# Kernel optimization log

Hardware: AMD Instinct MI355X
Metric: run time of the kernel (lower is better)

## Reference

```python
import jax, jax.numpy as jnp
import numpy as np

B, S, E, NH = 4, 1024, 512, 8
D = E // NH

def layer_norm(x, scale, bias, eps=1e-5):
    mu = jnp.mean(x, -1, keepdims=True)
    var = jnp.mean((x - mu) ** 2, -1, keepdims=True)
    return (x - mu) * jax.lax.rsqrt(var + eps) * scale + bias

def mha(qx, kx, vx, qw, qb, kw, kb, vw, vb, ow, ob, temp):
    b, sq, e = qx.shape
    sk = kx.shape[1]
    q = (qx @ qw + qb).reshape(b, sq, NH, D)
    k = (kx @ kw + kb).reshape(b, sk, NH, D)
    v = (vx @ vw + vb).reshape(b, sk, NH, D)
    scores = jnp.einsum('bqhd,bkhd->bhqk', q, k) * (D ** -0.5) / temp
    w = jax.nn.softmax(scores, axis=-1)  # dropout is identity in eval mode
    o = jnp.einsum('bhqk,bkhd->bqhd', w, v).reshape(b, sq, e)
    return o @ ow + ob

def setup_inputs():
    key = jax.random.key(0)
    ks = jax.random.split(key, 10)
    sc = 0.02  # init scale for weights
    return {
        'body_feats': jax.random.normal(ks[0], (B, S, E), jnp.float32),
        'limb_feats': jax.random.normal(ks[1], (B, S, E), jnp.float32),
        'attn_qw': jax.random.normal(ks[2], (4, E, E), jnp.float32) * sc,
        'attn_qb': jnp.zeros((4, E), jnp.float32),
        'attn_kw': jax.random.normal(ks[3], (4, E, E), jnp.float32) * sc,
        'attn_kb': jnp.zeros((4, E), jnp.float32),
        'attn_vw': jax.random.normal(ks[4], (4, E, E), jnp.float32) * sc,
        'attn_vb': jnp.zeros((4, E), jnp.float32),
        'attn_ow': jax.random.normal(ks[5], (4, E, E), jnp.float32) * sc,
        'attn_ob': jnp.zeros((4, E), jnp.float32),
        'ffn_w1': jax.random.normal(ks[6], (2, E, 4 * E), jnp.float32) * sc,
        'ffn_b1': jnp.zeros((2, 4 * E), jnp.float32),
        'ffn_w2': jax.random.normal(ks[7], (2, 4 * E, E), jnp.float32) * sc,
        'ffn_b2': jnp.zeros((2, E), jnp.float32),
        'norm_scale': jnp.ones((6, E), jnp.float32),
        'norm_bias': jnp.zeros((6, E), jnp.float32),
        'gate_w': jax.random.normal(ks[8], (2 * E, 2), jnp.float32) * sc,
        'gate_b': jnp.zeros((2,), jnp.float32),
        'temperature': 1,
    }

def reference(body_feats, limb_feats, attn_qw, attn_qb, attn_kw, attn_kb, attn_vw, attn_vb, attn_ow, attn_ob, ffn_w1, ffn_b1, ffn_w2, ffn_b2, norm_scale, norm_bias, gate_w, gate_b, temperature):
    temp = jnp.float32(temperature)
    # attn index: 0=self_body 1=self_limb 2=body2limb 3=limb2body
    # norm index: 0=norm1_body 1=norm2_body 2=norm3_body 3=norm1_limb 4=norm2_limb 5=norm3_limb
    def attn(i, qx, kx, vx):
        return mha(qx, kx, vx, attn_qw[i], attn_qb[i], attn_kw[i], attn_kb[i], attn_vw[i], attn_vb[i], attn_ow[i], attn_ob[i], temp)
    def ffn(i, x):
        return jax.nn.gelu(x @ ffn_w1[i] + ffn_b1[i], approximate=False) @ ffn_w2[i] + ffn_b2[i]
    def ln(i, x):
        return layer_norm(x, norm_scale[i], norm_bias[i])
    body = ln(0, body_feats + attn(0, body_feats, body_feats, body_feats))
    limb = ln(3, limb_feats + attn(1, limb_feats, limb_feats, limb_feats))
    body_cross = attn(2, body, limb, limb)
    limb_cross = attn(3, limb, body, body)
    body_gate = jax.nn.softmax(jnp.concatenate([body, body_cross], -1) @ gate_w + gate_b, axis=-1)
    limb_gate = jax.nn.softmax(jnp.concatenate([limb, limb_cross], -1) @ gate_w + gate_b, axis=-1)
    # NOTE: original torch code applies norm2_body to BOTH streams (preserved faithfully)
    body = ln(1, body * body_gate[..., 0:1] + body_cross * body_gate[..., 1:2])
    limb = ln(1, limb * limb_gate[..., 0:1] + limb_cross * limb_gate[..., 1:2])
    body = ln(2, body + ffn(0, body))
    limb = ln(5, limb + ffn(1, limb))
    return body, limb
```

## Files before the change

kernel.cpp:

```cpp
#include <hip/hip_runtime.h>

#define AS1 __attribute__((address_space(1)))
#define AS3 __attribute__((address_space(3)))

typedef __attribute__((ext_vector_type(4))) float f32x4;
typedef __attribute__((ext_vector_type(8))) short s16x8;

static __device__ __forceinline__ ushort f2bf(float f) {
  union { float f; unsigned u; } x; x.f = f;
  unsigned r = x.u + 0x7FFFu + ((x.u >> 16) & 1u);
  return (ushort)(r >> 16);
}
static __device__ __forceinline__ float bf2f(ushort u) {
  union { unsigned u; float f; } x; x.u = ((unsigned)u) << 16; return x.f;
}
static __device__ __forceinline__ float ex2(float x) {
  return __builtin_amdgcn_exp2f(x);
}
static __device__ __forceinline__ float parse_scalar(const void* p) {
  int i = *(const int*)p;
  if (i > 0 && i < 1000000) return (float)i;
  union { int i; float f; } u; u.i = i; return u.f;
}

__global__ __launch_bounds__(256)
void transpose_all(const float* __restrict__ qw, const float* __restrict__ kw,
                   const float* __restrict__ vw, const float* __restrict__ ow,
                   const float* __restrict__ w1, const float* __restrict__ w2,
                   ushort* __restrict__ FW, ushort* __restrict__ WOT,
                   ushort* __restrict__ W1T, ushort* __restrict__ W2T)
{
  __shared__ float tile[32][33];
  int id = blockIdx.x;
  const float* in; ushort* out; int K, N, tx, ty;
  if (id < 3072) {
    int trip = id / 768, r = id - trip * 768, which = r >> 8, t2 = r & 255;
    int widx = (which == 0) ? trip : (trip ^ (trip >> 1));
    in = ((which == 0) ? qw : (which == 1) ? kw : vw) + (size_t)widx * 512 * 512;
    out = FW + (size_t)trip * 1536 * 512 + (size_t)which * 512 * 512;
    K = 512; N = 512; tx = t2 & 15; ty = t2 >> 4;
  } else if (id < 4096) {
    int r = id - 3072, wi = r >> 8, t2 = r & 255;
    in = ow + (size_t)wi * 512 * 512; out = WOT + (size_t)wi * 512 * 512;
    K = 512; N = 512; tx = t2 & 15; ty = t2 >> 4;
  } else if (id < 6144) {
    int r = id - 4096, s = r >> 10, t2 = r & 1023;
    in = w1 + (size_t)s * 512 * 2048; out = W1T + (size_t)s * 2048 * 512;
    K = 512; N = 2048; tx = t2 & 63; ty = t2 >> 6;
  } else {
    int r = id - 6144, s = r >> 10, t2 = r & 1023;
    in = w2 + (size_t)s * 2048 * 512; out = W2T + (size_t)s * 512 * 2048;
    K = 2048; N = 512; tx = t2 & 15; ty = t2 >> 4;
  }
  int nb = tx * 32, kb = ty * 32;
  int x = threadIdx.x, y = threadIdx.y;
  #pragma unroll
  for (int i = 0; i < 4; ++i)
    tile[y + i * 8][x] = in[(size_t)(kb + y + i * 8) * N + nb + x];
  __syncthreads();
  #pragma unroll
  for (int i = 0; i < 4; ++i)
    out[(size_t)(nb + y + i * 8) * K + kb + x] = f2bf(tile[x][y + i * 8]);
}

__global__ __launch_bounds__(256)
void cvt2_bf16(const float* __restrict__ a, const float* __restrict__ b,
               ushort* __restrict__ oa, ushort* __restrict__ ob)
{
  const float* in = blockIdx.y ? b : a;
  ushort* out = blockIdx.y ? ob : oa;
  int i = (blockIdx.x * 256 + threadIdx.x) * 4;
  float4 v = *(const float4*)(in + i);
  ushort4 o;
  o.x = f2bf(v.x); o.y = f2bf(v.y); o.z = f2bf(v.z); o.w = f2bf(v.w);
  *(ushort4*)(out + i) = o;
}

struct GemmArgs {
  const ushort* A; const ushort* Bt;
  const float *b0, *b1, *b2;
  float* outf; ushort* outb;
  ushort *qo, *ko, *vto;
  const void* sp;
  int M, N, K, kind;
};

template<int FM, int FN>
__global__ __launch_bounds__(256)
void gemm_k(GemmArgs g0, GemmArgs g1)
{
  constexpr int BM = FM * 32, BN = FN * 32;
  __shared__ ushort As[2][BM * 64];
  __shared__ ushort Bs[2][BN * 64];
  GemmArgs g = blockIdx.z ? g1 : g0;
  const int t = threadIdx.x, lane = t & 63, w = t >> 6;
  const int lr = lane & 15, gq = lane >> 4;
  const int wr = w >> 1, wc = w & 1;
  const int m0 = blockIdx.y * BM, n0 = blockIdx.x * BN;
  const int K = g.K;
  const int nk = K >> 6;

  auto stage = [&](int kt, int buf) {
    #pragma unroll
    for (int p = 0; p < FM; ++p) {
      int c = p * 256 + t, row = c >> 3, sl = c & 7;
      const ushort* src = g.A + (size_t)(m0 + row) * K + kt * 64 + ((sl ^ (row & 7)) << 3);
      __builtin_amdgcn_global_load_lds((const AS1 void*)src,
          (AS3 void*)(As[buf] + (size_t)(p * 256 + (t & ~63)) * 8), 16, 0, 0);
    }
    #pragma unroll
    for (int p = 0; p < FN; ++p) {
      int c = p * 256 + t, row = c >> 3, sl = c & 7;
      const ushort* src = g.Bt + (size_t)(n0 + row) * K + kt * 64 + ((sl ^ (row & 7)) << 3);
      __builtin_amdgcn_global_load_lds((const AS1 void*)src,
          (AS3 void*)(Bs[buf] + (size_t)(p * 256 + (t & ~63)) * 8), 16, 0, 0);
    }
  };

  f32x4 acc[FM][FN];
  f32x4 zero = {0.f, 0.f, 0.f, 0.f};
  #pragma unroll
  for (int m = 0; m < FM; ++m)
    #pragma unroll
    for (int n = 0; n < FN; ++n) acc[m][n] = zero;

  stage(0, 0);
  __syncthreads();
  for (int kt = 0; kt < nk; ++kt) {
    int cur = kt & 1;
    const ushort* Ab = As[cur];
    const ushort* Bb = Bs[cur];
    if (kt + 1 < nk) stage(kt + 1, cur ^ 1);
    #pragma unroll
    for (int ks = 0; ks < 2; ++ks) {
      s16x8 af[FM], bfv[FN];
      #pragma unroll
      for (int m = 0; m < FM; ++m) {
        int row = wr * (FM * 16) + m * 16 + lr;
        af[m] = *(const s16x8*)(Ab + row * 64 + (((ks * 4 + gq) ^ (row & 7)) << 3));
      }
      #pragma unroll
      for (int n = 0; n < FN; ++n) {
        int row = wc * (FN * 16) + n * 16 + lr;
        bfv[n] = *(const s16x8*)(Bb + row * 64 + (((ks * 4 + gq) ^ (row & 7)) << 3));
      }
      __builtin_amdgcn_s_setprio(1);
      #pragma unroll
      for (int m = 0; m < FM; ++m)
        #pragma unroll
        for (int n = 0; n < FN; ++n)
          acc[m][n] = __builtin_amdgcn_mfma_f32_16x16x32_bf16(af[m], bfv[n], acc[m][n], 0, 0, 0);
      __builtin_amdgcn_s_setprio(0);
    }
    __syncthreads();
  }

  float qs = 1.0f;
  if (g.kind == 3 && g.sp) qs = 0.125f / parse_scalar(g.sp) * 1.4426950408889634f;
  #pragma unroll
  for (int n = 0; n < FN; ++n) {
    int col = n0 + wc * (FN * 16) + n * 16 + lr;
    int seg = col >> 9, cm = col & 511;
    float bv;
    if (g.kind == 3) bv = (seg == 0) ? g.b0[cm] : (seg == 1) ? g.b1[cm] : g.b2[cm];
    else bv = g.b0 ? g.b0[col] : 0.f;
    #pragma unroll
    for (int m = 0; m < FM; ++m) {
      int rowb = m0 + wr * (FM * 16) + m * 16 + 4 * gq;
      if (g.kind == 3) {
        if (seg == 2) {
          int d = cm & 63, hh = cm >> 6, bb = rowb >> 10, s = rowb & 1023;
          ushort4 pk;
          pk.x = f2bf(acc[m][n][0] + bv); pk.y = f2bf(acc[m][n][1] + bv);
          pk.z = f2bf(acc[m][n][2] + bv); pk.w = f2bf(acc[m][n][3] + bv);
          *(ushort4*)(g.vto + (((size_t)(bb * 8 + hh) * 64 + d) << 10) + s) = pk;
        } else if (seg == 1) {
          #pragma unroll
          for (int r = 0; r < 4; ++r)
            g.ko[(size_t)(rowb + r) * 512 + cm] = f2bf(acc[m][n][r] + bv);
        } else {
          #pragma unroll
          for (int r = 0; r < 4; ++r)
            g.qo[(size_t)(rowb + r) * 512 + cm] = f2bf((acc[m][n][r] + bv) * qs);
        }
      } else {
        #pragma unroll
        for (int r = 0; r < 4; ++r) {
          float v = acc[m][n][r] + bv;
          if (g.kind == 2) v = 0.5f * v * (1.0f + erff(v * 0.70710678118654752f));
          if (g.kind == 0) g.outf[(size_t)(rowb + r) * g.N + col] = v;
          else g.outb[(size_t)(rowb + r) * g.N + col] = f2bf(v);
        }
      }
    }
  }
}

__global__ __launch_bounds__(256)
void attn_core(const ushort* __restrict__ Q0, const ushort* __restrict__ K0,
               const ushort* __restrict__ V0, ushort* __restrict__ O0,
               const ushort* __restrict__ Q1, const ushort* __restrict__ K1,
               const ushort* __restrict__ V1, ushort* __restrict__ O1)
{
  __shared__ ushort Ks[2][64 * 64];
  __shared__ ushort Vs[2][64 * 64];
  __shared__ ushort Ps[4][1024];
  const int str = blockIdx.y;
  const ushort* Q = str ? Q1 : Q0;
  const ushort* Kx = str ? K1 : K0;
  const ushort* VT = str ? V1 : V0;
  ushort* O = str ? O1 : O0;

  const int t = threadIdx.x, lane = t & 63, w = t >> 6;
  const int lr = lane & 15, g = lane >> 4;
  int bid = blockIdx.x;
  int L = (bid & 7) * 64 + (bid >> 3);
  int bh = L >> 4, qt = L & 15;
  size_t tbase = ((size_t)(bh >> 3) << 19) + ((size_t)(bh & 7) << 6);
  const ushort* Kbase = Kx + tbase;
  const ushort* Vbase = VT + ((size_t)bh << 16);
  int q0 = qt * 64 + w * 16;
  ushort* myPs = Ps[w];

  auto stage = [&](int kt, int buf) {
    #pragma unroll
    for (int p = 0; p < 2; ++p) {
      int c = p * 256 + t, row = c >> 3, sl = c & 7;
      const ushort* src = Kbase + (size_t)(kt * 64 + row) * 512 + ((sl ^ (row & 7)) << 3);
      __builtin_amdgcn_global_load_lds((const AS1 void*)src,
          (AS3 void*)(Ks[buf] + (size_t)(p * 256 + (t & ~63)) * 8), 16, 0, 0);
    }
    #pragma unroll
    for (int p = 0; p < 2; ++p) {
      int c = p * 256 + t, row = c >> 3, sl = c & 7;
      const ushort* src = Vbase + (size_t)row * 1024 + kt * 64 + ((sl ^ (row & 7)) << 3);
      __builtin_amdgcn_global_load_lds((const AS1 void*)src,
          (AS3 void*)(Vs[buf] + (size_t)(p * 256 + (t & ~63)) * 8), 16, 0, 0);
    }
  };

  s16x8 qf[2];
  #pragma unroll
  for (int ks = 0; ks < 2; ++ks)
    qf[ks] = *(const s16x8*)(Q + tbase + (size_t)(q0 + lr) * 512 + ks * 32 + g * 8);

  f32x4 po[4];
  f32x4 zero = {0.f, 0.f, 0.f, 0.f};
  #pragma unroll
  for (int dt = 0; dt < 4; ++dt) po[dt] = zero;
  float mrow[4] = {-1e30f, -1e30f, -1e30f, -1e30f};
  float lsum[4] = {0.f, 0.f, 0.f, 0.f};

  stage(0, 0);
  __syncthreads();
  #pragma unroll 2
  for (int kt = 0; kt < 16; ++kt) {
    int cur = kt & 1;
    const ushort* Kb = Ks[cur];
    const ushort* Vb = Vs[cur];
    if (kt < 15) stage(kt + 1, cur ^ 1);

    f32x4 sc[4];
    #pragma unroll
    for (int c = 0; c < 4; ++c) {
      sc[c] = zero;
      #pragma unroll
      for (int ks = 0; ks < 2; ++ks) {
        int row = c * 16 + lr;
        s16x8 kf = *(const s16x8*)(Kb + row * 64 + (((ks * 4 + g) ^ (row & 7)) << 3));
        sc[c] = __builtin_amdgcn_mfma_f32_16x16x32_bf16(qf[ks], kf, sc[c], 0, 0, 0);
      }
    }

    #pragma unroll
    for (int r = 0; r < 4; ++r) {
      float tm = fmaxf(fmaxf(sc[0][r], sc[1][r]), fmaxf(sc[2][r], sc[3][r]));
      #pragma unroll
      for (int msk = 1; msk < 16; msk <<= 1) tm = fmaxf(tm, __shfl_xor(tm, msk));
      float nm = fmaxf(mrow[r], tm);
      float fr = ex2(mrow[r] - nm);
      float ps = 0.f;
      #pragma unroll
      for (int c = 0; c < 4; ++c) {
        float pv = ex2(sc[c][r] - nm);
        sc[c][r] = pv;
        ps += pv;
      }
      #pragma unroll
      for (int msk = 1; msk < 16; msk <<= 1) ps += __shfl_xor(ps, msk);
      lsum[r] = lsum[r] * fr + ps;
      mrow[r] = nm;
      #pragma unroll
      for (int dt = 0; dt < 4; ++dt) po[dt][r] *= fr;
    }

    #pragma unroll
    for (int c = 0; c < 4; ++c)
      #pragma unroll
      for (int r = 0; r < 4; ++r) {
        int qq = 4 * g + r;
        int pa = (qq * 128 + (c * 16 + lr) * 2) ^ ((qq & 7) << 4);
        *(ushort*)((char*)myPs + pa) = f2bf(sc[c][r]);
      }
    s16x8 paf[2];
    #pragma unroll
    for (int ks = 0; ks < 2; ++ks)
      paf[ks] = *(const s16x8*)((char*)myPs + ((lr * 128 + ks * 64 + g * 16) ^ ((lr & 7) << 4)));
    __builtin_amdgcn_s_setprio(1);
    #pragma unroll
    for (int dt = 0; dt < 4; ++dt) {
      int vrow0 = dt * 16 + lr;
      #pragma unroll
      for (int ks = 0; ks < 2; ++ks) {
        s16x8 vf = *(const s16x8*)(Vb + vrow0 * 64 + (((ks * 4 + g) ^ (vrow0 & 7)) << 3));
        po[dt] = __builtin_amdgcn_mfma_f32_16x16x32_bf16(paf[ks], vf, po[dt], 0, 0, 0);
      }
    }
    __builtin_amdgcn_s_setprio(0);
    __syncthreads();
  }

  #pragma unroll
  for (int r = 0; r < 4; ++r) {
    float inv = 1.0f / lsum[r];
    #pragma unroll
    for (int dt = 0; dt < 4; ++dt)
      O[tbase + (size_t)(q0 + 4 * g + r) * 512 + dt * 16 + lr] = f2bf(po[dt][r] * inv);
  }
}

__global__ __launch_bounds__(256)
void add_ln_ff2(const float* __restrict__ a0, const float* __restrict__ b0,
                ushort* __restrict__ o0, const float* __restrict__ a1,
                const float* __restrict__ b1, ushort* __restrict__ o1,
                const float* __restrict__ nsc, const float* __restrict__ nbi,
                int i0, int i1)
{
  const float* a = blockIdx.y ? a1 : a0;
  const float* b = blockIdx.y ? b1 : b0;
  ushort* outb = blockIdx.y ? o1 : o0;
  const float* scale = nsc + (blockIdx.y ? i1 : i0) * 512;
  const float* bias = nbi + (blockIdx.y ? i1 : i0) * 512;
  const int lane = threadIdx.x & 63, w = threadIdx.x >> 6;
  const size_t row = blockIdx.x * 4 + w;
  float x[8];
  #pragma unroll
  for (int j = 0; j < 8; j += 4) {
    float4 av = *(const float4*)(a + row * 512 + lane * 8 + j);
    float4 bv = *(const float4*)(b + row * 512 + lane * 8 + j);
    x[j] = av.x + bv.x; x[j + 1] = av.y + bv.y;
    x[j + 2] = av.z + bv.z; x[j + 3] = av.w + bv.w;
  }
  float s = 0.f, ss = 0.f;
  #pragma unroll
  for (int j = 0; j < 8; ++j) { s += x[j]; ss += x[j] * x[j]; }
  #pragma unroll
  for (int m = 1; m < 64; m <<= 1) { s += __shfl_xor(s, m); ss += __shfl_xor(ss, m); }
  float mu = s * (1.f / 512.f);
  float rstd = rsqrtf(ss * (1.f / 512.f) - mu * mu + 1e-5f);
  ushort o[8];
  #pragma unroll
  for (int j = 0; j < 8; ++j) {
    int e = lane * 8 + j;
    o[j] = f2bf((x[j] - mu) * rstd * scale[e] + bias[e]);
  }
  *(s16x8*)(outb + row * 512 + lane * 8) = *(s16x8*)o;
}

__global__ __launch_bounds__(256)
void add_ln_bf2(const ushort* __restrict__ a0, const float* __restrict__ b0,
                float* __restrict__ o0, const ushort* __restrict__ a1,
                const float* __restrict__ b1, float* __restrict__ o1,
                const float* __restrict__ nsc, const float* __restrict__ nbi,
                int i0, int i1)
{
  const ushort* a = blockIdx.y ? a1 : a0;
  const float* b = blockIdx.y ? b1 : b0;
  float* outf = blockIdx.y ? o1 : o0;
  const float* scale = nsc + (blockIdx.y ? i1 : i0) * 512;
  const float* bias = nbi + (blockIdx.y ? i1 : i0) * 512;
  const int lane = threadIdx.x & 63, w = threadIdx.x >> 6;
  const size_t row = blockIdx.x * 4 + w;
  s16x8 av = *(const s16x8*)(a + row * 512 + lane * 8);
  float x[8];
  #pragma unroll
  for (int j = 0; j < 8; j += 4) {
    float4 bv = *(const float4*)(b + row * 512 + lane * 8 + j);
    x[j] = bf2f((ushort)av[j]) + bv.x; x[j + 1] = bf2f((ushort)av[j + 1]) + bv.y;
    x[j + 2] = bf2f((ushort)av[j + 2]) + bv.z; x[j + 3] = bf2f((ushort)av[j + 3]) + bv.w;
  }
  float s = 0.f, ss = 0.f;
  #pragma unroll
  for (int j = 0; j < 8; ++j) { s += x[j]; ss += x[j] * x[j]; }
  #pragma unroll
  for (int m = 1; m < 64; m <<= 1) { s += __shfl_xor(s, m); ss += __shfl_xor(ss, m); }
  float mu = s * (1.f / 512.f);
  float rstd = rsqrtf(ss * (1.f / 512.f) - mu * mu + 1e-5f);
  float o[8];
  #pragma unroll
  for (int j = 0; j < 8; ++j) {
    int e = lane * 8 + j;
    o[j] = (x[j] - mu) * rstd * scale[e] + bias[e];
  }
  *(float4*)(outf + row * 512 + lane * 8) = *(float4*)o;
  *(float4*)(outf + row * 512 + lane * 8 + 4) = *(float4*)(o + 4);
}

__global__ __launch_bounds__(256)
void gate_ln2(const ushort* __restrict__ x0, const ushort* __restrict__ c0,
              ushort* __restrict__ o0, const ushort* __restrict__ x1,
              const ushort* __restrict__ c1, ushort* __restrict__ o1,
              const float* __restrict__ gw, const float* __restrict__ gb,
              const float* __restrict__ scale, const float* __restrict__ bias)
{
  const ushort* x = blockIdx.y ? x1 : x0;
  const ushort* cr = blockIdx.y ? c1 : c0;
  ushort* outb = blockIdx.y ? o1 : o0;
  const int lane = threadIdx.x & 63, w = threadIdx.x >> 6;
  const size_t row = blockIdx.x * 4 + w;
  s16x8 xv8 = *(const s16x8*)(x + row * 512 + lane * 8);
  s16x8 cv8 = *(const s16x8*)(cr + row * 512 + lane * 8);
  float xv[8], cv[8];
  #pragma unroll
  for (int j = 0; j < 8; ++j) { xv[j] = bf2f((ushort)xv8[j]); cv[j] = bf2f((ushort)cv8[j]); }
  float d0 = 0.f, d1 = 0.f;
  #pragma unroll
  for (int j = 0; j < 8; ++j) {
    int e = lane * 8 + j;
    float2 g0 = *(const float2*)(gw + 2 * e);
    float2 g1 = *(const float2*)(gw + 2 * (512 + e));
    d0 += xv[j] * g0.x + cv[j] * g1.x;
    d1 += xv[j] * g0.y + cv[j] * g1.y;
  }
  #pragma unroll
  for (int m = 1; m < 64; m <<= 1) { d0 += __shfl_xor(d0, m); d1 += __shfl_xor(d1, m); }
  d0 += gb[0]; d1 += gb[1];
  float mx = fmaxf(d0, d1);
  float e0 = __expf(d0 - mx), e1 = __expf(d1 - mx);
  float inv = 1.0f / (e0 + e1);
  float g0w = e0 * inv, g1w = e1 * inv;
  float xc[8];
  float s = 0.f, ss = 0.f;
  #pragma unroll
  for (int j = 0; j < 8; ++j) {
    xc[j] = xv[j] * g0w + cv[j] * g1w;
    s += xc[j]; ss += xc[j] * xc[j];
  }
  #pragma unroll
  for (int m = 1; m < 64; m <<= 1) { s += __shfl_xor(s, m); ss += __shfl_xor(ss, m); }
  float mu = s * (1.f / 512.f);
  float rstd = rsqrtf(ss * (1.f / 512.f) - mu * mu + 1e-5f);
  ushort o[8];
  #pragma unroll
  for (int j = 0; j < 8; ++j) {
    int e = lane * 8 + j;
    o[j] = f2bf((xc[j] - mu) * rstd * scale[e] + bias[e]);
  }
  *(s16x8*)(outb + row * 512 + lane * 8) = *(s16x8*)o;
}

extern "C" void kernel_launch(void* const* d_in, const int* in_sizes, int n_in,
                              void* d_out, int out_size, void* d_ws, size_t ws_size,
                              hipStream_t stream)
{
  (void)in_sizes; (void)n_in; (void)out_size; (void)ws_size;
  const int T = 4096, E = 512, HD = 2048;
  const float* body = (const float*)d_in[0];
  const float* limb = (const float*)d_in[1];
  const float* qw = (const float*)d_in[2];  const float* qb = (const float*)d_in[3];
  const float* kw = (const float*)d_in[4];  const float* kb = (const float*)d_in[5];
  const float* vw = (const float*)d_in[6];  const float* vb = (const float*)d_in[7];
  const float* ow = (const float*)d_in[8];  const float* ob = (const float*)d_in[9];
  const float* w1 = (const float*)d_in[10]; const float* fb1 = (const float*)d_in[11];
  const float* w2 = (const float*)d_in[12]; const float* fb2 = (const float*)d_in[13];
  const float* nsc = (const float*)d_in[14]; const float* nbi = (const float*)d_in[15];
  const float* gw = (const float*)d_in[16];  const float* gb = (const float*)d_in[17];
  const void* temp = d_in[18];

  char* ws = (char*)d_ws;
  size_t off = 0;
  auto alloc = [&](size_t b) { char* p = ws + off; off += (b + 255) & ~(size_t)255; return p; };
  ushort* FW    = (ushort*)alloc((size_t)4 * 1536 * 512 * 2);
  ushort* WOT   = (ushort*)alloc((size_t)4 * E * E * 2);
  ushort* W1T   = (ushort*)alloc((size_t)2 * E * HD * 2);
  ushort* W2T   = (ushort*)alloc((size_t)2 * HD * E * 2);
  ushort* XB    = (ushort*)alloc((size_t)T * E * 2);
  ushort* XL    = (ushort*)alloc((size_t)T * E * 2);
  float*  PROJA = (float*)alloc((size_t)T * E * 4);
  float*  PROJB = (float*)alloc((size_t)T * E * 4);
  ushort* BODYb = (ushort*)alloc((size_t)T * E * 2);
  ushort* LIMBb = (ushort*)alloc((size_t)T * E * 2);
  ushort* BCRb  = (ushort*)alloc((size_t)T * E * 2);
  ushort* LCRb  = (ushort*)alloc((size_t)T * E * 2);
  ushort* GBb   = (ushort*)alloc((size_t)T * E * 2);
  ushort* GLb   = (ushort*)alloc((size_t)T * E * 2);
  ushort* QA    = (ushort*)alloc((size_t)T * E * 2);
  ushort* KA    = (ushort*)alloc((size_t)T * E * 2);
  ushort* VTA   = (ushort*)alloc((size_t)T * E * 2);
  ushort* QB    = (ushort*)alloc((size_t)T * E * 2);
  ushort* KB    = (ushort*)alloc((size_t)T * E * 2);
  ushort* VTB   = (ushort*)alloc((size_t)T * E * 2);
  ushort* AOA   = (ushort*)alloc((size_t)T * E * 2);
  ushort* AOB   = (ushort*)alloc((size_t)T * E * 2);
  ushort* H1A   = QA;
  ushort* H1B   = KB;
  float*  FFNA  = PROJA;
  float*  FFNB  = PROJB;

  transpose_all<<<8192, dim3(32, 8), 0, stream>>>(qw, kw, vw, ow, w1, w2, FW, WOT, W1T, W2T);
  cvt2_bf16<<<dim3(T * E / 1024, 2), 256, 0, stream>>>(body, limb, XB, XL);

  auto qkv_pair = [&](const ushort* A0, int t0, ushort* q0, ushort* k0, ushort* v0,
                      const ushort* A1, int t1, ushort* q1, ushort* k1, ushort* v1) {
    GemmArgs a{}, b{};
    int kv0 = t0 ^ (t0 >> 1), kv1 = t1 ^ (t1 >> 1);
    a.A = A0; a.Bt = FW + (size_t)t0 * 1536 * 512;
    a.b0 = qb + t0 * E; a.b1 = kb + kv0 * E; a.b2 = vb + kv0 * E;
    a.qo = q0; a.ko = k0; a.vto = v0; a.sp = temp; a.M = T; a.N = 1536; a.K = E; a.kind = 3;
    b = a;
    b.A = A1; b.Bt = FW + (size_t)t1 * 1536 * 512;
    b.b0 = qb + t1 * E; b.b1 = kb + kv1 * E; b.b2 = vb + kv1 * E;
    b.qo = q1; b.ko = k1; b.vto = v1;
    gemm_k<4, 4><<<dim3(12, 32, 2), 256, 0, stream>>>(a, b);
  };
  auto oproj_pair = [&](const ushort* A0, int i0, float* of0, ushort* ob0,
                        const ushort* A1, int i1, float* of1, ushort* ob1, int kind) {
    GemmArgs a{}, b{};
    a.A = A0; a.Bt = WOT + (size_t)i0 * E * E; a.b0 = ob + i0 * E;
    a.outf = of0; a.outb = ob0; a.M = T; a.N = E; a.K = E; a.kind = kind;
    b = a;
    b.A = A1; b.Bt = WOT + (size_t)i1 * E * E; b.b0 = ob + i1 * E;
    b.outf = of1; b.outb = ob1;
    gemm_k<2, 4><<<dim3(4, 64, 2), 256, 0, stream>>>(a, b);
  };

  qkv_pair(XB, 0, QA, KA, VTA, XL, 1, QB, KB, VTB);
  attn_core<<<dim3(512, 2), 256, 0, stream>>>(QA, KA, VTA, AOA, QB, KB, VTB, AOB);
  oproj_pair(AOA, 0, PROJA, nullptr, AOB, 1, PROJB, nullptr, 0);
  add_ln_ff2<<<dim3(T / 4, 2), 256, 0, stream>>>(body, PROJA, BODYb, limb, PROJB, LIMBb,
                                                 nsc, nbi, 0, 3);
  qkv_pair(BODYb, 2, QA, KA, VTA, LIMBb, 3, QB, KB, VTB);
  attn_core<<<dim3(512, 2), 256, 0, stream>>>(QA, KB, VTB, AOA, QB, KA, VTA, AOB);
  oproj_pair(AOA, 2, nullptr, BCRb, AOB, 3, nullptr, LCRb, 1);

  gate_ln2<<<dim3(T / 4, 2), 256, 0, stream>>>(BODYb, BCRb, GBb, LIMBb, LCRb, GLb,
                                               gw, gb, nsc + E, nbi + E);

  {
    GemmArgs a{}, b{};
    a.A = GBb; a.Bt = W1T; a.b0 = fb1; a.outb = H1A;
    a.M = T; a.N = HD; a.K = E; a.kind = 2;
    b = a; b.A = GLb; b.Bt = W1T + (size_t)HD * E; b.b0 = fb1 + HD; b.outb = H1B;
    gemm_k<4, 4><<<dim3(16, 32, 2), 256, 0, stream>>>(a, b);
  }
  {
    GemmArgs a{}, b{};
    a.A = H1A; a.Bt = W2T; a.b0 = fb2; a.outf = FFNA;
    a.M = T; a.N = E; a.K = HD; a.kind = 0;
    b = a; b.A = H1B; b.Bt = W2T + (size_t)HD * E; b.b0 = fb2 + E; b.outf = FFNB;
    gemm_k<2, 4><<<dim3(4, 64, 2), 256, 0, stream>>>(a, b);
  }
  add_ln_bf2<<<dim3(T / 4, 2), 256, 0, stream>>>(GBb, FFNA, (float*)d_out,
                                                 GLb, FFNB, (float*)d_out + (size_t)T * E,
                                                 nsc, nbi, 2, 5);
}
```

Measured before the change: 454.4 us.

## Swap MFMA operand order so each lane owns one query row in attention

Swaps the A/B operands of both attention MFMAs so the score and output accumulators are transposed, putting one query row per lane column. Row max and sum then reduce mostly within a lane, needing only two cross-lane shuffles instead of four per row for each of four rows, and the online-softmax state shrinks to one scalar per lane. P is written to LDS with packed bf16 conversions as 8-byte stores, and the output is written as 4-element vector stores. This cuts shuffle, conversion and store instruction counts in the inner loop. The bf16 rounding now comes from the hardware packed convert, which may differ slightly from the software rounding path.

```diff
diff --git a/kernel.cpp b/kernel.cpp
--- a/kernel.cpp
+++ b/kernel.cpp
@@ -16,6 +16,11 @@
 }
 static __device__ __forceinline__ float ex2(float x) {
   return __builtin_amdgcn_exp2f(x);
+}
+static __device__ __forceinline__ unsigned cvt_pk_bf16(float a, float b) {
+  unsigned r;
+  asm("v_cvt_pk_bf16_f32 %0, %1, %2" : "=v"(r) : "v"(a), "v"(b));
+  return r;
 }
 static __device__ __forceinline__ float parse_scalar(const void* p) {
   int i = *(const int*)p;
@@ -220,7 +225,8 @@
   const ushort* Kbase = Kx + tbase;
   const ushort* Vbase = VT + ((size_t)bh << 16);
   int q0 = qt * 64 + w * 16;
-  ushort* myPs = Ps[w];
+  char* myPs = (char*)Ps[w];
+  const int psw = (lr & 7) << 4;
 
   auto stage = [&](int kt, int buf) {
     #pragma unroll
@@ -248,8 +254,7 @@
   f32x4 zero = {0.f, 0.f, 0.f, 0.f};
   #pragma unroll
   for (int dt = 0; dt < 4; ++dt) po[dt] = zero;
-  float mrow[4] = {-1e30f, -1e30f, -1e30f, -1e30f};
-  float lsum[4] = {0.f, 0.f, 0.f, 0.f};
+  float mrow = -1e30f, lsum = 0.f;
 
   stage(0, 0);
   __syncthreads();
@@ -268,64 +273,70 @@
       for (int ks = 0; ks < 2; ++ks) {
         int row = c * 16 + lr;
         s16x8 kf = *(const s16x8*)(Kb + row * 64 + (((ks * 4 + g) ^ (row & 7)) << 3));
-        sc[c] = __builtin_amdgcn_mfma_f32_16x16x32_bf16(qf[ks], kf, sc[c], 0, 0, 0);
+        sc[c] = __builtin_amdgcn_mfma_f32_16x16x32_bf16(kf, qf[ks], sc[c], 0, 0, 0);
       }
     }
 
-    #pragma unroll
-    for (int r = 0; r < 4; ++r) {
-      float tm = fmaxf(fmaxf(sc[0][r], sc[1][r]), fmaxf(sc[2][r], sc[3][r]));
-      #pragma unroll
-      for (int msk = 1; msk < 16; msk <<= 1) tm = fmaxf(tm, __shfl_xor(tm, msk));
-      float nm = fmaxf(mrow[r], tm);
-      float fr = ex2(mrow[r] - nm);
-      float ps = 0.f;
-      #pragma unroll
-      for (int c = 0; c < 4; ++c) {
+    float tm = sc[0][0];
+    #pragma unroll
+    for (int c = 0; c < 4; ++c)
+      #pragma unroll
+      for (int r = 0; r < 4; ++r) tm = fmaxf(tm, sc[c][r]);
+    tm = fmaxf(tm, __shfl_xor(tm, 16));
+    tm = fmaxf(tm, __shfl_xor(tm, 32));
+    float nm = fmaxf(mrow, tm);
+    float fr = ex2(mrow - nm);
+    float ts = 0.f;
+    #pragma unroll
+    for (int c = 0; c < 4; ++c)
+      #pragma unroll
+      for (int r = 0; r < 4; ++r) {
         float pv = ex2(sc[c][r] - nm);
         sc[c][r] = pv;
-        ps += pv;
+        ts += pv;
       }
-      #pragma unroll
-      for (int msk = 1; msk < 16; msk <<= 1) ps += __shfl_xor(ps, msk);
-      lsum[r] = lsum[r] * fr + ps;
-      mrow[r] = nm;
-      #pragma unroll
-      for (int dt = 0; dt < 4; ++dt) po[dt][r] *= fr;
-    }
-
-    #pragma unroll
-    for (int c = 0; c < 4; ++c)
-      #pragma unroll
-      for (int r = 0; r < 4; ++r) {
-        int qq = 4 * g + r;
-        int pa = (qq * 128 + (c * 16 + lr) * 2) ^ ((qq & 7) << 4);
-        *(ushort*)((char*)myPs + pa) = f2bf(sc[c][r]);
-      }
+    ts += __shfl_xor(ts, 16);
+    ts += __shfl_xor(ts, 32);
+    lsum = lsum * fr + ts;
+    mrow = nm;
+    #pragma unroll
+    for (int dt = 0; dt < 4; ++dt) po[dt] *= fr;
+
+    #pragma unroll
+    for (int c = 0; c < 4; ++c) {
+      uint2 d;
+      d.x = cvt_pk_bf16(sc[c][0], sc[c][1]);
+      d.y = cvt_pk_bf16(sc[c][2], sc[c][3]);
+      *(uint2*)(myPs + lr * 128 + ((c * 32 + g * 8) ^ psw)) = d;
+    }
     s16x8 paf[2];
     #pragma unroll
     for (int ks = 0; ks < 2; ++ks)
-      paf[ks] = *(const s16x8*)((char*)myPs + ((lr * 128 + ks * 64 + g * 16) ^ ((lr & 7) << 4)));
+      paf[ks] = *(const s16x8*)(myPs + lr * 128 + ((ks * 64 + g * 16) ^ psw));
+
     __builtin_amdgcn_s_setprio(1);
     #pragma unroll
     for (int dt = 0; dt < 4; ++dt) {
-      int vrow0 = dt * 16 + lr;
+      int vrow = dt * 16 + lr;
       #pragma unroll
       for (int ks = 0; ks < 2; ++ks) {
-        s16x8 vf = *(const s16x8*)(Vb + vrow0 * 64 + (((ks * 4 + g) ^ (vrow0 & 7)) << 3));
-        po[dt] = __builtin_amdgcn_mfma_f32_16x16x32_bf16(paf[ks], vf, po[dt], 0, 0, 0);
+        s16x8 vf = *(const s16x8*)(Vb + vrow * 64 + (((ks * 4 + g) ^ (vrow & 7)) << 3));
+        po[dt] = __builtin_amdgcn_mfma_f32_16x16x32_bf16(vf, paf[ks], po[dt], 0, 0, 0);
       }
     }
     __builtin_amdgcn_s_setprio(0);
     __syncthreads();
   }
 
-  #pragma unroll
-  for (int r = 0; r < 4; ++r) {
-    float inv = 1.0f / lsum[r];
-    #pragma unroll
-    for (int dt = 0; dt < 4; ++dt)
-      O[tbase + (size_t)(q0 + 4 * g + r) * 512 + dt * 16 + lr] = f2bf(po[dt][r] * inv);
+  float inv = 1.0f / lsum;
+  #pragma unroll
+  for (int dt = 0; dt < 4; ++dt) {
+    ushort4 pk;
+    pk.x = f2bf(po[dt][0] * inv);
+    pk.y = f2bf(po[dt][1] * inv);
+    pk.z = f2bf(po[dt][2] * inv);
+    pk.w = f2bf(po[dt][3] * inv);
+    *(ushort4*)(O + tbase + (size_t)(q0 + lr) * 512 + dt * 16 + 4 * g) = pk;
   }
 }
 
```

New measurement: 404.1 us. 11.1% less time.
